# Kernel optimization log

Hardware: AMD Instinct MI355X
Metric: run time of the kernel (lower is better)

Reference implementation:

```python
import jax, jax.numpy as jnp
import numpy as np

EPS = 0.1        # init kwarg: eps
MAX_ITER = 50    # init kwarg: max_iter
EPS_LOG = 1e-8


def setup_inputs() -> dict:
    key = jax.random.key(0)
    k1, k2 = jax.random.split(key)
    x = jax.random.uniform(k1, (8, 2048, 2), dtype=jnp.float32)
    y = jax.random.uniform(k2, (8, 2048, 2), dtype=jnp.float32)
    return {"x": x, "y": y}


def _cost_matrix(x, y):
    # |x_i - y_j|^2 summed over feature dim -> (N, P, P)
    return jnp.sum(jnp.abs(x[:, :, None, :] - y[:, None, :, :]) ** 2, axis=-1)


def _M(C, u, v):
    # modified cost for log-domain updates: (-C + u_i + v_j) / eps
    return (-C + u[..., :, None] + v[..., None, :]) / EPS


def reference(x, y):
    mask = (x != -1).astype(x.dtype)
    x = x * mask
    y = y * mask

    C = _cost_matrix(x, y)  # (N, P, P)

    # marginals from squared second coordinate (detached in the original)
    a = x[:, :, 1] ** 2 / jnp.sum(x[:, :, 1] ** 2, axis=1, keepdims=True)
    b = y[:, :, 1] ** 2 / jnp.sum(y[:, :, 1] ** 2, axis=1, keepdims=True)
    mu = jax.lax.stop_gradient(a)
    nu = jax.lax.stop_gradient(b)

    u = jnp.zeros_like(mu)
    v = jnp.zeros_like(nu)

    def step(carry, _):
        u, v = carry
        u = EPS * (jnp.log(mu + EPS_LOG) - jax.nn.logsumexp(_M(C, u, v), axis=-1)) + u
        # logsumexp over transposed M == reduce over axis=-2
        v = EPS * (jnp.log(nu + EPS_LOG) - jax.nn.logsumexp(_M(C, u, v), axis=-2)) + v
        return (u, v), None

    (u, v), _ = jax.lax.scan(step, (u, v), None, length=MAX_ITER)

    pi = jnp.exp(_M(C, u, v))                 # transport plan (N, P, P)
    cost = jnp.sum(pi * C, axis=(-2, -1))     # (N,), reduction='none'
    return cost, pi, C
```

## Files before the change

kernel.cpp:

```cpp
#include <hip/hip_runtime.h>
#include <hip/hip_bf16.h>


#define P 2048
#define NB 8
constexpr float SCALE = 14.426950408889634f;

typedef float vf4 __attribute__((ext_vector_type(4)));

__global__ void setup_kernel(const float* __restrict__ x, const float* __restrict__ yy,
                             float4* __restrict__ jpackY, float4* __restrict__ jpackX,
                             float4* __restrict__ rowX, float4* __restrict__ rowY,
                             float* __restrict__ u, float* __restrict__ v,
                             float* __restrict__ partial) {
    const int n = blockIdx.x;
    const int t = threadIdx.x;
    __shared__ float redx[256], redy[256];
    float xm0[8], xm1[8], ym0[8], ym1[8];
    float sx = 0.f, sy = 0.f;
    #pragma unroll
    for (int k = 0; k < 8; ++k) {
        int p = t + 256 * k;
        size_t base = ((size_t)n * P + p) * 2;
        float a0 = x[base + 0];
        float a1 = x[base + 1];
        float b0 = yy[base + 0];
        float b1 = yy[base + 1];
        float m0 = (a0 != -1.0f) ? 1.0f : 0.0f;
        float m1 = (a1 != -1.0f) ? 1.0f : 0.0f;
        a0 *= m0; a1 *= m1; b0 *= m0; b1 *= m1;
        xm0[k] = a0; xm1[k] = a1; ym0[k] = b0; ym1[k] = b1;
        sx = fmaf(a1, a1, sx);
        sy = fmaf(b1, b1, sy);
    }
    redx[t] = sx; redy[t] = sy;
    __syncthreads();
    for (int off = 128; off > 0; off >>= 1) {
        if (t < off) { redx[t] += redx[t + off]; redy[t] += redy[t + off]; }
        __syncthreads();
    }
    const float inv_sx = 1.0f / redx[0];
    const float inv_sy = 1.0f / redy[0];
    #pragma unroll
    for (int k = 0; k < 8; ++k) {
        int p = t + 256 * k;
        float a0 = xm0[k], a1 = xm1[k], b0 = ym0[k], b1 = ym1[k];
        float qx = fmaf(a0, a0, a1 * a1);
        float qy = fmaf(b0, b0, b1 * b1);
        float mu = a1 * a1 * inv_sx;
        float nu = b1 * b1 * inv_sy;
        float Bmu = __builtin_amdgcn_logf(mu + 1e-8f) + SCALE * qx;
        float Bnu = __builtin_amdgcn_logf(nu + 1e-8f) + SCALE * qy;
        size_t idx = (size_t)n * P + p;
        rowX[idx] = make_float4(a0, a1, Bmu, 0.f);
        rowY[idx] = make_float4(b0, b1, Bnu, 0.f);
        jpackX[idx] = make_float4(2.f * SCALE * a0, 2.f * SCALE * a1, SCALE * qx, 0.f);
        jpackY[idx] = make_float4(2.f * SCALE * b0, 2.f * SCALE * b1, SCALE * qy, 0.f);
        u[idx] = 0.f;
        v[idx] = 0.f;
    }
    if (n == 0) { partial[t] = 0.f; partial[t + 256] = 0.f; }
}

__global__ __launch_bounds__(256, 2) void halfpass_kernel(
        const float4* __restrict__ jpack, const float* __restrict__ jdual,
        const float4* __restrict__ rowdat, float* __restrict__ outdual) {
    const int blk = blockIdx.x;
    const int batch = blk & 7;
    const int blkin = blk >> 3;
    const int lane = threadIdx.x & 63;
    const int wave = threadIdx.x >> 6;

    const float4* jp = jpack + (size_t)batch * P;
    const float* jd = jdual + (size_t)batch * P;

    float Y0[32], Y1[32], V[32];
    #pragma unroll
    for (int k = 0; k < 32; ++k) {
        int j = lane + 64 * k;
        float4 q = jp[j];
        float dv = jd[j];
        Y0[k] = q.x;
        Y1[k] = q.y;
        V[k] = dv - q.z;
    }

    const int rowbase = blkin * 32 + wave * 8;
    const float4* rd = rowdat + (size_t)batch * P;
    float* outp = outdual + (size_t)batch * P;

    for (int r = 0; r < 8; ++r) {
        const int i = rowbase + r;
        float4 rv = rd[i];
        const float x0 = rv.x, x1 = rv.y, B = rv.z;
        float a0 = 0.f, a1 = 0.f, a2 = 0.f, a3 = 0.f;
        #pragma unroll
        for (int k = 0; k < 32; k += 4) {
            a0 += __builtin_amdgcn_exp2f(fmaf(Y1[k + 0], x1, fmaf(Y0[k + 0], x0, V[k + 0])));
            a1 += __builtin_amdgcn_exp2f(fmaf(Y1[k + 1], x1, fmaf(Y0[k + 1], x0, V[k + 1])));
            a2 += __builtin_amdgcn_exp2f(fmaf(Y1[k + 2], x1, fmaf(Y0[k + 2], x0, V[k + 2])));
            a3 += __builtin_amdgcn_exp2f(fmaf(Y1[k + 3], x1, fmaf(Y0[k + 3], x0, V[k + 3])));
        }
        float acc = (a0 + a1) + (a2 + a3);
        #pragma unroll
        for (int m = 1; m < 64; m <<= 1) acc += __shfl_xor(acc, m, 64);
        if (lane == 0) outp[i] = B - __builtin_amdgcn_logf(acc);
    }
}

__global__ void final_kernel(const float4* __restrict__ rowX, const float4* __restrict__ rowY,
                             const float* __restrict__ u, const float* __restrict__ v,
                             float* __restrict__ out, float* __restrict__ partial) {
    const int blk = blockIdx.x;
    const int batch = blk & 7;
    const int i = blk >> 3;
    const int t = threadIdx.x;

    const float4 rx = rowX[(size_t)batch * P + i];
    const float ui = u[(size_t)batch * P + i];
    const float x0 = rx.x, x1 = rx.y;

    float* pi_out = out + 8 + (size_t)batch * P * P + (size_t)i * P;
    float* C_out = pi_out + (size_t)NB * P * P;
    const float4* ry = rowY + (size_t)batch * P;
    const float* vv = v + (size_t)batch * P;

    float costacc = 0.f;
    #pragma unroll
    for (int c = 0; c < 2; ++c) {
        const int j0 = c * 1024 + t * 4;
        vf4 vj = *(const vf4*)(vv + j0);
        vf4 Cv, Pv;
        #pragma unroll
        for (int e = 0; e < 4; ++e) {
            float4 q = ry[j0 + e];
            float dx = x0 - q.x;
            float dy = x1 - q.y;
            float Cj = fmaf(dy, dy, dx * dx);
            float pj = __builtin_amdgcn_exp2f(fmaf(Cj, -SCALE, ui + vj[e]));
            Cv[e] = Cj;
            Pv[e] = pj;
            costacc = fmaf(pj, Cj, costacc);
        }
        __builtin_nontemporal_store(Pv, (vf4*)(pi_out + j0));
        __builtin_nontemporal_store(Cv, (vf4*)(C_out + j0));
    }

    #pragma unroll
    for (int m = 1; m < 64; m <<= 1) costacc += __shfl_xor(costacc, m, 64);
    __shared__ float sred[4];
    const int wave = t >> 6, lane = t & 63;
    if (lane == 0) sred[wave] = costacc;
    __syncthreads();
    if (t == 0) {
        float s = sred[0] + sred[1] + sred[2] + sred[3];
        atomicAdd(&partial[batch * 64 + (i & 63)], s);
    }
}

__global__ void costreduce_kernel(const float* __restrict__ partial, float* __restrict__ out) {
    const int t = threadIdx.x;
    float val = partial[t];
    #pragma unroll
    for (int m = 1; m < 64; m <<= 1) val += __shfl_xor(val, m, 64);
    if ((t & 63) == 0) out[t >> 6] = val;
}

extern "C" void kernel_launch(void* const* d_in, const int* in_sizes, int n_in,
                              void* d_out, int out_size, void* d_ws, size_t ws_size,
                              hipStream_t stream) {
    const float* x = (const float*)d_in[0];
    const float* y = (const float*)d_in[1];
    float* out = (float*)d_out;
    float* ws = (float*)d_ws;

    float4* jpackY = (float4*)ws;
    float4* jpackX = (float4*)(ws + 65536);
    float4* rowX = (float4*)(ws + 131072);
    float4* rowY = (float4*)(ws + 196608);
    float* u = ws + 262144;
    float* v = ws + 262144 + 16384;
    float* partial = ws + 262144 + 32768;

    setup_kernel<<<8, 256, 0, stream>>>(x, y, jpackY, jpackX, rowX, rowY, u, v, partial);
    for (int it = 0; it < 50; ++it) {
        halfpass_kernel<<<512, 256, 0, stream>>>(jpackY, v, rowX, u);
        halfpass_kernel<<<512, 256, 0, stream>>>(jpackX, u, rowY, v);
    }
    final_kernel<<<16384, 256, 0, stream>>>(rowX, rowY, u, v, out, partial);
    costreduce_kernel<<<1, 512, 0, stream>>>(partial, out);
}
```

Baseline: 1.307 ms.

## Fuse all Sinkhorn iterations into one persistent kernel with per-batch grid barriers

Replaces the 100 separate half-pass launches with a single persistent kernel. It keeps both X and Y coordinate sets in registers and synchronises the 64 blocks of each batch through atomic-counter spin barriers. The dual vectors are now read with contiguous vector loads, the squared-norm term is recomputed from the register coordinates, and the packed coordinate buffers shrink to float2. The goal is to remove launch overhead and repeated coordinate reloads. The cost is higher register pressure and reliance on all 512 blocks being co-resident, otherwise the spin barrier can deadlock until its guard expires.

Result: slower. 3.408 ms (+160.7%).

```diff
diff --git a/kernel.cpp b/kernel.cpp
--- a/kernel.cpp
+++ b/kernel.cpp
@@ -1,18 +1,19 @@
 #include <hip/hip_runtime.h>
-#include <hip/hip_bf16.h>
 
 
 #define P 2048
 #define NB 8
 constexpr float SCALE = 14.426950408889634f;
+constexpr float INV4S = 1.0f / (4.0f * SCALE);
 
 typedef float vf4 __attribute__((ext_vector_type(4)));
 
+
 __global__ void setup_kernel(const float* __restrict__ x, const float* __restrict__ yy,
-                             float4* __restrict__ jpackY, float4* __restrict__ jpackX,
+                             float2* __restrict__ jpY, float2* __restrict__ jpX,
                              float4* __restrict__ rowX, float4* __restrict__ rowY,
                              float* __restrict__ u, float* __restrict__ v,
-                             float* __restrict__ partial) {
+                             float* __restrict__ partial, unsigned* __restrict__ bar) {
     const int n = blockIdx.x;
     const int t = threadIdx.x;
     __shared__ float redx[256], redy[256];
@@ -54,57 +55,120 @@
         size_t idx = (size_t)n * P + p;
         rowX[idx] = make_float4(a0, a1, Bmu, 0.f);
         rowY[idx] = make_float4(b0, b1, Bnu, 0.f);
-        jpackX[idx] = make_float4(2.f * SCALE * a0, 2.f * SCALE * a1, SCALE * qx, 0.f);
-        jpackY[idx] = make_float4(2.f * SCALE * b0, 2.f * SCALE * b1, SCALE * qy, 0.f);
+        jpX[idx] = make_float2(2.f * SCALE * a0, 2.f * SCALE * a1);
+        jpY[idx] = make_float2(2.f * SCALE * b0, 2.f * SCALE * b1);
         u[idx] = 0.f;
         v[idx] = 0.f;
     }
-    if (n == 0) { partial[t] = 0.f; partial[t + 256] = 0.f; }
-}
-
-__global__ __launch_bounds__(256, 2) void halfpass_kernel(
-        const float4* __restrict__ jpack, const float* __restrict__ jdual,
-        const float4* __restrict__ rowdat, float* __restrict__ outdual) {
+    if (n == 0) {
+        partial[t] = 0.f; partial[t + 256] = 0.f;
+        if (t < 8) bar[t] = 0u;
+    }
+}
+
+__device__ __forceinline__ void batch_barrier(unsigned* bar, unsigned target) {
+    __syncthreads();
+    if (threadIdx.x == 0) {
+        __hip_atomic_fetch_add(bar, 1u, __ATOMIC_RELEASE, __HIP_MEMORY_SCOPE_AGENT);
+        int guard = 0;
+        while (__hip_atomic_load(bar, __ATOMIC_RELAXED, __HIP_MEMORY_SCOPE_AGENT) < target) {
+            __builtin_amdgcn_s_sleep(2);
+            if (++guard > (1 << 22)) break;
+        }
+        (void)__hip_atomic_load(bar, __ATOMIC_ACQUIRE, __HIP_MEMORY_SCOPE_AGENT);
+    }
+    __syncthreads();
+}
+
+__device__ __forceinline__ float rowsum(const float (&Y0)[32], const float (&Y1)[32],
+                                        const float (&V)[32], float x0, float x1) {
+    float a0 = 0.f, a1 = 0.f, a2 = 0.f, a3 = 0.f;
+    #pragma unroll
+    for (int k = 0; k < 32; k += 4) {
+        a0 += __builtin_amdgcn_exp2f(fmaf(Y1[k + 0], x1, fmaf(Y0[k + 0], x0, V[k + 0])));
+        a1 += __builtin_amdgcn_exp2f(fmaf(Y1[k + 1], x1, fmaf(Y0[k + 1], x0, V[k + 1])));
+        a2 += __builtin_amdgcn_exp2f(fmaf(Y1[k + 2], x1, fmaf(Y0[k + 2], x0, V[k + 2])));
+        a3 += __builtin_amdgcn_exp2f(fmaf(Y1[k + 3], x1, fmaf(Y0[k + 3], x0, V[k + 3])));
+    }
+    return (a0 + a1) + (a2 + a3);
+}
+
+__device__ __forceinline__ void half_phase(const float (&Y0)[32], const float (&Y1)[32],
+                                           const float* __restrict__ din,
+                                           const float4* __restrict__ rdat,
+                                           float* __restrict__ dout,
+                                           const int lane, const int rowbase) {
+    float V[32];
+    const vf4* dp = (const vf4*)(din + (size_t)lane * 32);
+    #pragma unroll
+    for (int k8 = 0; k8 < 8; ++k8) {
+        vf4 d = dp[k8];
+        #pragma unroll
+        for (int e = 0; e < 4; ++e) {
+            int k = k8 * 4 + e;
+            float q = fmaf(Y0[k], Y0[k], Y1[k] * Y1[k]);
+            V[k] = fmaf(q, -INV4S, d[e]);
+        }
+    }
+    float acc[8], Bs[8];
+    #pragma unroll
+    for (int r = 0; r < 8; ++r) {
+        float4 rv = rdat[rowbase + r];
+        Bs[r] = rv.z;
+        acc[r] = rowsum(Y0, Y1, V, rv.x, rv.y);
+    }
+    #pragma unroll
+    for (int r = 0; r < 8; ++r) {
+        float a = acc[r];
+        #pragma unroll
+        for (int m = 1; m < 64; m <<= 1) a += __shfl_xor(a, m, 64);
+        acc[r] = a;
+    }
+    if (lane == 0) {
+        #pragma unroll
+        for (int r = 0; r < 8; ++r)
+            dout[rowbase + r] = Bs[r] - __builtin_amdgcn_logf(acc[r]);
+    }
+}
+
+__global__ __launch_bounds__(256, 2) void sinkhorn_iter_kernel(
+        const float2* __restrict__ jpY, const float2* __restrict__ jpX,
+        const float4* __restrict__ rowX, const float4* __restrict__ rowY,
+        float* __restrict__ u, float* __restrict__ v, unsigned* __restrict__ bar) {
     const int blk = blockIdx.x;
     const int batch = blk & 7;
     const int blkin = blk >> 3;
     const int lane = threadIdx.x & 63;
     const int wave = threadIdx.x >> 6;
-
-    const float4* jp = jpack + (size_t)batch * P;
-    const float* jd = jdual + (size_t)batch * P;
-
-    float Y0[32], Y1[32], V[32];
-    #pragma unroll
-    for (int k = 0; k < 32; ++k) {
-        int j = lane + 64 * k;
-        float4 q = jp[j];
-        float dv = jd[j];
-        Y0[k] = q.x;
-        Y1[k] = q.y;
-        V[k] = dv - q.z;
-    }
-
     const int rowbase = blkin * 32 + wave * 8;
-    const float4* rd = rowdat + (size_t)batch * P;
-    float* outp = outdual + (size_t)batch * P;
-
-    for (int r = 0; r < 8; ++r) {
-        const int i = rowbase + r;
-        float4 rv = rd[i];
-        const float x0 = rv.x, x1 = rv.y, B = rv.z;
-        float a0 = 0.f, a1 = 0.f, a2 = 0.f, a3 = 0.f;
-        #pragma unroll
-        for (int k = 0; k < 32; k += 4) {
-            a0 += __builtin_amdgcn_exp2f(fmaf(Y1[k + 0], x1, fmaf(Y0[k + 0], x0, V[k + 0])));
-            a1 += __builtin_amdgcn_exp2f(fmaf(Y1[k + 1], x1, fmaf(Y0[k + 1], x0, V[k + 1])));
-            a2 += __builtin_amdgcn_exp2f(fmaf(Y1[k + 2], x1, fmaf(Y0[k + 2], x0, V[k + 2])));
-            a3 += __builtin_amdgcn_exp2f(fmaf(Y1[k + 3], x1, fmaf(Y0[k + 3], x0, V[k + 3])));
-        }
-        float acc = (a0 + a1) + (a2 + a3);
-        #pragma unroll
-        for (int m = 1; m < 64; m <<= 1) acc += __shfl_xor(acc, m, 64);
-        if (lane == 0) outp[i] = B - __builtin_amdgcn_logf(acc);
+
+    const float2* jY = jpY + (size_t)batch * P;
+    const float2* jX = jpX + (size_t)batch * P;
+    const float4* rX = rowX + (size_t)batch * P;
+    const float4* rY = rowY + (size_t)batch * P;
+    float* ub = u + (size_t)batch * P;
+    float* vb = v + (size_t)batch * P;
+    unsigned* mybar = bar + batch;
+
+    float Yy0[32], Yy1[32], Yx0[32], Yx1[32];
+    const vf4* py = (const vf4*)(jY + (size_t)lane * 32);
+    const vf4* px = (const vf4*)(jX + (size_t)lane * 32);
+    #pragma unroll
+    for (int m = 0; m < 16; ++m) {
+        vf4 qy = py[m];
+        vf4 qx = px[m];
+        Yy0[2 * m] = qy[0]; Yy1[2 * m] = qy[1];
+        Yy0[2 * m + 1] = qy[2]; Yy1[2 * m + 1] = qy[3];
+        Yx0[2 * m] = qx[0]; Yx1[2 * m] = qx[1];
+        Yx0[2 * m + 1] = qx[2]; Yx1[2 * m + 1] = qx[3];
+    }
+
+    unsigned tgt = 0;
+    for (int it = 0; it < 50; ++it) {
+        half_phase(Yy0, Yy1, vb, rX, ub, lane, rowbase);
+        tgt += 64; batch_barrier(mybar, tgt);
+        half_phase(Yx0, Yx1, ub, rY, vb, lane, rowbase);
+        if (it < 49) { tgt += 64; batch_barrier(mybar, tgt); }
     }
 }
 
@@ -174,19 +238,17 @@
     float* out = (float*)d_out;
     float* ws = (float*)d_ws;
 
-    float4* jpackY = (float4*)ws;
-    float4* jpackX = (float4*)(ws + 65536);
-    float4* rowX = (float4*)(ws + 131072);
-    float4* rowY = (float4*)(ws + 196608);
-    float* u = ws + 262144;
-    float* v = ws + 262144 + 16384;
-    float* partial = ws + 262144 + 32768;
-
-    setup_kernel<<<8, 256, 0, stream>>>(x, y, jpackY, jpackX, rowX, rowY, u, v, partial);
-    for (int it = 0; it < 50; ++it) {
-        halfpass_kernel<<<512, 256, 0, stream>>>(jpackY, v, rowX, u);
-        halfpass_kernel<<<512, 256, 0, stream>>>(jpackX, u, rowY, v);
-    }
+    float2* jpY = (float2*)ws;
+    float2* jpX = (float2*)(ws + 32768);
+    float4* rowX = (float4*)(ws + 65536);
+    float4* rowY = (float4*)(ws + 131072);
+    float* u = ws + 196608;
+    float* v = ws + 196608 + 16384;
+    float* partial = ws + 196608 + 32768;
+    unsigned* bar = (unsigned*)(ws + 196608 + 32768 + 512);
+
+    setup_kernel<<<8, 256, 0, stream>>>(x, y, jpY, jpX, rowX, rowY, u, v, partial, bar);
+    sinkhorn_iter_kernel<<<512, 256, 0, stream>>>(jpY, jpX, rowX, rowY, u, v, bar);
     final_kernel<<<16384, 256, 0, stream>>>(rowX, rowY, u, v, out, partial);
     costreduce_kernel<<<1, 512, 0, stream>>>(partial, out);
 }
```

## Stage column data in LDS and process eight rows per wave concurrently

Applied to the files above, without the earlier changes.

Halfpass now loads the column coordinates and dual into shared memory once per block, instead of each wave holding 96 registers of column data. Each wave then sweeps the columns in chunks and accumulates all eight rows at once, so every LDS read is reused across eight rows. The squared-norm term is recomputed from the packed coordinates, which lets the packed column buffer shrink from float4 to float2, and the eight outputs are written as vector stores. The cost is LDS traffic and a block barrier in exchange for lower register pressure and more instruction-level parallelism in the exp2-bound inner loop.

Result: faster. 1.053 ms (-19.4%).

```diff
diff --git a/kernel.cpp b/kernel.cpp
--- a/kernel.cpp
+++ b/kernel.cpp
@@ -1,15 +1,16 @@
 #include <hip/hip_runtime.h>
-#include <hip/hip_bf16.h>
 
 
 #define P 2048
 #define NB 8
 constexpr float SCALE = 14.426950408889634f;
+constexpr float INV4S = 1.0f / (4.0f * SCALE);
 
 typedef float vf4 __attribute__((ext_vector_type(4)));
 
+
 __global__ void setup_kernel(const float* __restrict__ x, const float* __restrict__ yy,
-                             float4* __restrict__ jpackY, float4* __restrict__ jpackX,
+                             float2* __restrict__ jpY, float2* __restrict__ jpX,
                              float4* __restrict__ rowX, float4* __restrict__ rowY,
                              float* __restrict__ u, float* __restrict__ v,
                              float* __restrict__ partial) {
@@ -54,8 +55,8 @@
         size_t idx = (size_t)n * P + p;
         rowX[idx] = make_float4(a0, a1, Bmu, 0.f);
         rowY[idx] = make_float4(b0, b1, Bnu, 0.f);
-        jpackX[idx] = make_float4(2.f * SCALE * a0, 2.f * SCALE * a1, SCALE * qx, 0.f);
-        jpackY[idx] = make_float4(2.f * SCALE * b0, 2.f * SCALE * b1, SCALE * qy, 0.f);
+        jpX[idx] = make_float2(2.f * SCALE * a0, 2.f * SCALE * a1);
+        jpY[idx] = make_float2(2.f * SCALE * b0, 2.f * SCALE * b1);
         u[idx] = 0.f;
         v[idx] = 0.f;
     }
@@ -63,48 +64,79 @@
 }
 
 __global__ __launch_bounds__(256, 2) void halfpass_kernel(
-        const float4* __restrict__ jpack, const float* __restrict__ jdual,
+        const float2* __restrict__ jp, const float* __restrict__ jdual,
         const float4* __restrict__ rowdat, float* __restrict__ outdual) {
     const int blk = blockIdx.x;
     const int batch = blk & 7;
     const int blkin = blk >> 3;
-    const int lane = threadIdx.x & 63;
-    const int wave = threadIdx.x >> 6;
-
-    const float4* jp = jpack + (size_t)batch * P;
-    const float* jd = jdual + (size_t)batch * P;
-
-    float Y0[32], Y1[32], V[32];
-    #pragma unroll
-    for (int k = 0; k < 32; ++k) {
-        int j = lane + 64 * k;
-        float4 q = jp[j];
-        float dv = jd[j];
-        Y0[k] = q.x;
-        Y1[k] = q.y;
-        V[k] = dv - q.z;
-    }
+    const int t = threadIdx.x;
+    const int lane = t & 63;
+    const int wave = t >> 6;
+
+    __shared__ float Y0s[P];
+    __shared__ float Y1s[P];
+    __shared__ float Vs[P];
+
+    {
+        const float2* jpb = jp + (size_t)batch * P;
+        const float* ddb = jdual + (size_t)batch * P;
+        #pragma unroll
+        for (int c = 0; c < 8; ++c) {
+            int j = t + 256 * c;
+            float2 p = jpb[j];
+            float d = ddb[j];
+            float q = fmaf(p.x, p.x, p.y * p.y);
+            Y0s[j] = p.x;
+            Y1s[j] = p.y;
+            Vs[j] = fmaf(q, -INV4S, d);
+        }
+    }
+    __syncthreads();
 
     const int rowbase = blkin * 32 + wave * 8;
     const float4* rd = rowdat + (size_t)batch * P;
-    float* outp = outdual + (size_t)batch * P;
-
+    float x0[8], x1[8], Bs[8], acc[8];
+    #pragma unroll
     for (int r = 0; r < 8; ++r) {
-        const int i = rowbase + r;
-        float4 rv = rd[i];
-        const float x0 = rv.x, x1 = rv.y, B = rv.z;
-        float a0 = 0.f, a1 = 0.f, a2 = 0.f, a3 = 0.f;
-        #pragma unroll
-        for (int k = 0; k < 32; k += 4) {
-            a0 += __builtin_amdgcn_exp2f(fmaf(Y1[k + 0], x1, fmaf(Y0[k + 0], x0, V[k + 0])));
-            a1 += __builtin_amdgcn_exp2f(fmaf(Y1[k + 1], x1, fmaf(Y0[k + 1], x0, V[k + 1])));
-            a2 += __builtin_amdgcn_exp2f(fmaf(Y1[k + 2], x1, fmaf(Y0[k + 2], x0, V[k + 2])));
-            a3 += __builtin_amdgcn_exp2f(fmaf(Y1[k + 3], x1, fmaf(Y0[k + 3], x0, V[k + 3])));
-        }
-        float acc = (a0 + a1) + (a2 + a3);
-        #pragma unroll
-        for (int m = 1; m < 64; m <<= 1) acc += __shfl_xor(acc, m, 64);
-        if (lane == 0) outp[i] = B - __builtin_amdgcn_logf(acc);
+        float4 rv = rd[rowbase + r];
+        x0[r] = rv.x; x1[r] = rv.y; Bs[r] = rv.z;
+        acc[r] = 0.f;
+    }
+    #pragma unroll
+    for (int g = 0; g < 8; ++g) {
+        float cy0[4], cy1[4], cv[4];
+        #pragma unroll
+        for (int e = 0; e < 4; ++e) {
+            int j = (4 * g + e) * 64 + lane;
+            cy0[e] = Y0s[j];
+            cy1[e] = Y1s[j];
+            cv[e] = Vs[j];
+        }
+        #pragma unroll
+        for (int r = 0; r < 8; ++r) {
+            #pragma unroll
+            for (int e = 0; e < 4; ++e)
+                acc[r] += __builtin_amdgcn_exp2f(
+                    fmaf(cy1[e], x1[r], fmaf(cy0[e], x0[r], cv[e])));
+        }
+    }
+    #pragma unroll
+    for (int r = 0; r < 8; ++r) {
+        float a = acc[r];
+        #pragma unroll
+        for (int m = 1; m < 64; m <<= 1) a += __shfl_xor(a, m, 64);
+        acc[r] = a;
+    }
+    if (lane == 0) {
+        vf4 o0, o1;
+        #pragma unroll
+        for (int r = 0; r < 4; ++r) {
+            o0[r] = Bs[r] - __builtin_amdgcn_logf(acc[r]);
+            o1[r] = Bs[r + 4] - __builtin_amdgcn_logf(acc[r + 4]);
+        }
+        float* op = outdual + (size_t)batch * P + rowbase;
+        *(vf4*)op = o0;
+        *(vf4*)(op + 4) = o1;
     }
 }
 
@@ -174,18 +206,18 @@
     float* out = (float*)d_out;
     float* ws = (float*)d_ws;
 
-    float4* jpackY = (float4*)ws;
-    float4* jpackX = (float4*)(ws + 65536);
-    float4* rowX = (float4*)(ws + 131072);
-    float4* rowY = (float4*)(ws + 196608);
-    float* u = ws + 262144;
-    float* v = ws + 262144 + 16384;
-    float* partial = ws + 262144 + 32768;
-
-    setup_kernel<<<8, 256, 0, stream>>>(x, y, jpackY, jpackX, rowX, rowY, u, v, partial);
+    float2* jpY = (float2*)ws;
+    float2* jpX = (float2*)(ws + 32768);
+    float4* rowX = (float4*)(ws + 65536);
+    float4* rowY = (float4*)(ws + 131072);
+    float* u = ws + 196608;
+    float* v = ws + 196608 + 16384;
+    float* partial = ws + 196608 + 32768;
+
+    setup_kernel<<<8, 256, 0, stream>>>(x, y, jpY, jpX, rowX, rowY, u, v, partial);
     for (int it = 0; it < 50; ++it) {
-        halfpass_kernel<<<512, 256, 0, stream>>>(jpackY, v, rowX, u);
-        halfpass_kernel<<<512, 256, 0, stream>>>(jpackX, u, rowY, v);
+        halfpass_kernel<<<512, 256, 0, stream>>>(jpY, v, rowX, u);
+        halfpass_kernel<<<512, 256, 0, stream>>>(jpX, u, rowY, v);
     }
     final_kernel<<<16384, 256, 0, stream>>>(rowX, rowY, u, v, out, partial);
     costreduce_kernel<<<1, 512, 0, stream>>>(partial, out);
```
